# Performance work log

Hardware: AMD Instinct MI355X
Metric: run time of the kernel (lower is better)

Reference implementation:

```python
import jax, jax.numpy as jnp
import numpy as np

N_NODES = 50000
N_EDGES = 800000
D = 64
H = 128


def setup_inputs() -> dict:
    key = jax.random.key(0)
    ks = jax.random.split(key, 6)
    x = jax.random.normal(ks[0], (N_NODES, D), dtype=jnp.float32)
    edge_index = jax.random.randint(ks[1], (2, N_EDGES), 0, N_NODES, dtype=jnp.int64)
    # GIN MLP params (Linear(D->H) -> ReLU -> Linear(H->D))
    W1 = jax.random.normal(ks[2], (D, H), dtype=jnp.float32) * (1.0 / np.sqrt(D))
    b1 = jnp.zeros((H,), dtype=jnp.float32)
    W2 = jax.random.normal(ks[3], (H, D), dtype=jnp.float32) * (1.0 / np.sqrt(H))
    b2 = jnp.zeros((D,), dtype=jnp.float32)
    eps = jnp.zeros((1, 1), dtype=jnp.float32)  # trainable eps parameter
    return {"x": x, "W1": W1, "b1": b1, "W2": W2, "b2": b2, "eps": eps,
            "edge_index": edge_index}


def reference(x, W1, b1, W2, b2, eps, edge_index):
    src, dst = edge_index[0], edge_index[1]
    # node -> edge gather (0th-order ptensor on each edge = sum of endpoint feats)
    msg = x[src] + x[dst]                                    # [E, D]
    # edge -> node gather: each node sums messages of its incident edges
    agg = (jax.ops.segment_sum(msg, src, num_segments=N_NODES)
           + jax.ops.segment_sum(msg, dst, num_segments=N_NODES))  # [N, D]
    ones = jnp.ones((N_EDGES,), dtype=x.dtype)
    deg = (jax.ops.segment_sum(ones, src, num_segments=N_NODES)
           + jax.ops.segment_sum(ones, dst, num_segments=N_NODES))  # [N]
    # subtract deg*x so aggregation reduces to the plain neighbor sum (GIN)
    neighbor = agg - x * deg[:, None]
    out = (1.0 + eps) * x + neighbor                          # eps is [1,1], broadcasts
    # GIN MLP
    h = jax.nn.relu(out @ W1 + b1)
    return h @ W2 + b2
```

## Files before the change

kernel.cpp:

```cpp
#include <hip/hip_runtime.h>


#define D 64
#define H 128
#define MPW 8
#define REGSH 6
#define REGSZ 64
#define P1_BLOCKS 256
#define EVBUF_SZ 6400
#define NR_MAX 1024
#define NCAP 96

typedef __attribute__((ext_vector_type(8))) short short8;
typedef __attribute__((ext_vector_type(4))) float float4v;

__device__ __forceinline__ float lane_bcast(float v, int l) {
    return __uint_as_float(__builtin_amdgcn_readlane(__float_as_uint(v), l));
}

__device__ __forceinline__ unsigned short f2bf(float f) {
    unsigned int u = __float_as_uint(f);
    u = (u + (((u >> 16) & 1u) + 0x7fffu)) >> 16;
    return (unsigned short)u;
}

__device__ __forceinline__ void bf2_acc(unsigned int u, float& a, float& b) {
    a += __uint_as_float(u << 16);
    b += __uint_as_float(u & 0xffff0000u);
}

__global__ void zero_int_kernel(int* __restrict__ p, int n) {
    int i = blockIdx.x * blockDim.x + threadIdx.x;
    if (i < n) p[i] = 0;
}

__global__ void zero_f_kernel(float* __restrict__ p, int n) {
    int i = blockIdx.x * blockDim.x + threadIdx.x;
    if (i < n) p[i] = 0.0f;
}

__global__ void prep_kernel(const float* __restrict__ x,
                            unsigned int* __restrict__ xh2, int npairs,
                            int* __restrict__ cursor, int NR, int CAPB,
                            const float* __restrict__ W1,
                            const float* __restrict__ W2,
                            unsigned short* __restrict__ wsW1,
                            unsigned short* __restrict__ wsW2) {
    int i = blockIdx.x * blockDim.x + threadIdx.x;
    int gs = gridDim.x * blockDim.x;
    for (int k = i; k < npairs; k += gs) {
        float2 v = *(const float2*)(x + (size_t)k * 2);
        unsigned int a = __float_as_uint(v.x);
        unsigned int b = __float_as_uint(v.y);
        a = (a + (((a >> 16) & 1u) + 0x7fffu)) >> 16;
        b = (b + (((b >> 16) & 1u) + 0x7fffu)) >> 16;
        xh2[k] = a | (b << 16);
    }
    if (i < NR) cursor[i] = i * CAPB;
    if (i < 32) xh2[npairs + i] = 0;
    if (i < 8192) {
        int j = i & 7, ln = (i >> 3) & 63;
        int q = (ln >> 4) & 3;
        int tt1 = (i >> 9) & 7, s1 = i >> 12;
        wsW1[i] = f2bf(W1[(s1 * 32 + q * 8 + j) * H + tt1 * 16 + (ln & 15)]);
        int tt2 = (i >> 9) & 3, s2 = i >> 11;
        wsW2[i] = f2bf(W2[(s2 * 32 + q * 8 + j) * D + tt2 * 16 + (ln & 15)]);
    }
}

__global__ __launch_bounds__(256) void part1_kernel(
    const int* __restrict__ src, const int* __restrict__ dst,
    int* __restrict__ cursor, unsigned int* __restrict__ evarr,
    int E, int N, int NR, int CAPB, int EPB)
{
    __shared__ unsigned int evbuf[EVBUF_SZ];
    __shared__ int hist[NR_MAX];
    int t = threadIdx.x;
    for (int b = t; b < NR; b += 256) hist[b] = 0;
    __syncthreads();

    int e0 = blockIdx.x * EPB;
    int ne = E - e0; if (ne > EPB) ne = EPB; if (ne < 0) ne = 0;
    for (int i = t; i < ne; i += 256) {
        int s = src[e0 + i], d = dst[e0 + i];
        s = (s < 0) ? 0 : ((s >= N) ? N - 1 : s);
        d = (d < 0) ? 0 : ((d >= N) ? N - 1 : d);
        evbuf[2 * i]     = ((unsigned int)s << 16) | (unsigned int)d;
        evbuf[2 * i + 1] = ((unsigned int)d << 16) | (unsigned int)s;
        atomicAdd(&hist[s >> REGSH], 1);
        atomicAdd(&hist[d >> REGSH], 1);
    }
    __syncthreads();

    for (int b = t; b < NR; b += 256) {
        int c = hist[b];
        hist[b] = c ? atomicAdd(&cursor[b], c) : 0;
    }
    __syncthreads();

    int nev = 2 * ne;
    for (int i = t; i < nev; i += 256) {
        unsigned int ev = evbuf[i];
        int b = (int)(ev >> (16 + REGSH));
        int slot = atomicAdd(&hist[b], 1);
        if (slot < (b + 1) * CAPB) evarr[slot] = ev;
    }
}

__global__ __launch_bounds__(512) void part2_kernel(
    const unsigned int* __restrict__ evarr, const int* __restrict__ cursor,
    const unsigned short* __restrict__ xh, const float* __restrict__ x,
    const float* __restrict__ epsp, float* __restrict__ pre, int N, int CAPB)
{
    __shared__ unsigned short nbuf[REGSZ * NCAP + 32];
    __shared__ int scnt[REGSZ];
    int t = threadIdx.x;
    int b = blockIdx.x;
    if (t < REGSZ) scnt[t] = 0;
    __syncthreads();

    int base = b * CAPB;
    int count = cursor[b] - base;
    if (count < 0) count = 0;
    if (count > CAPB) count = CAPB;

    for (int i = t; i < count; i += 512) {
        unsigned int ev = evarr[base + i];
        int row = (int)((ev >> 16) & (REGSZ - 1));
        int k = atomicAdd(&scnt[row], 1);
        if (k < NCAP) nbuf[row * NCAP + k] = (unsigned short)(ev & 0xffffu);
    }
    __syncthreads();

    int wave = t >> 6, lane = t & 63;
    int r = lane >> 5;
    int h = lane & 31;
    float e1 = 1.0f + epsp[0];

    for (int k = 0; k < 8; ++k) {
        int n = wave * 8 + k;
        int v = b * REGSZ + n;
        if (v >= N) break;
        int m = scnt[n]; m = (m > NCAP) ? NCAP : m;
        float f0 = 0.0f, f1 = 0.0f;
        for (int j = 0; j < m; j += 32) {
            int cc[16];
#pragma unroll
            for (int q = 0; q < 16; ++q) {
                int ii = j + 2 * q + r;
                int c = (int)nbuf[n * NCAP + ii];
                cc[q] = (ii < m) ? c : N;
            }
            unsigned int u[16];
#pragma unroll
            for (int q = 0; q < 16; ++q)
                u[q] = *(const unsigned int*)(xh + (size_t)cc[q] * D + 2 * h);
#pragma unroll
            for (int q = 0; q < 16; ++q) bf2_acc(u[q], f0, f1);
        }
        f0 += __shfl_xor(f0, 32, 64);
        f1 += __shfl_xor(f1, 32, 64);
        if (r == 0) {
            float2 sv = *(const float2*)(x + (size_t)v * D + 2 * h);
            float2 o;
            o.x = f0 + e1 * sv.x;
            o.y = f1 + e1 * sv.y;
            *(float2*)(pre + (size_t)v * D + 2 * h) = o;
        }
    }
}

__global__ __launch_bounds__(1024) void mlp_mfma(
    const float* __restrict__ pre,
    const unsigned short* __restrict__ wsW1,
    const unsigned short* __restrict__ wsW2,
    const float* __restrict__ b1, const float* __restrict__ b2,
    float* __restrict__ y, int N)
{
    __shared__ unsigned short sW1[8192];
    __shared__ unsigned short sW2[8192];
    __shared__ unsigned short hbuf[16 * 2048];
    int t = threadIdx.x;
    if (t < 1024) {
        ((uint4*)sW1)[t] = ((const uint4*)wsW1)[t];
        ((uint4*)sW2)[t] = ((const uint4*)wsW2)[t];
    }
    __syncthreads();

    int wave = t >> 6, lane = t & 63;
    int quad = lane >> 4, lm = lane & 15;
    int v0 = (blockIdx.x * 16 + wave) * 16;
    int vA = v0 + lm;

    short8 a1[2];
#pragma unroll
    for (int s = 0; s < 2; ++s) {
        float4v p0 = {0.f, 0.f, 0.f, 0.f}, p1 = {0.f, 0.f, 0.f, 0.f};
        if (vA < N) {
            const float* rp = pre + (size_t)vA * D + s * 32 + quad * 8;
            p0 = *(const float4v*)rp;
            p1 = *(const float4v*)(rp + 4);
        }
        short8 a;
        a[0] = (short)f2bf(p0[0]); a[1] = (short)f2bf(p0[1]);
        a[2] = (short)f2bf(p0[2]); a[3] = (short)f2bf(p0[3]);
        a[4] = (short)f2bf(p1[0]); a[5] = (short)f2bf(p1[1]);
        a[6] = (short)f2bf(p1[2]); a[7] = (short)f2bf(p1[3]);
        a1[s] = a;
    }

    float4v acc1[8];
#pragma unroll
    for (int tt = 0; tt < 8; ++tt) {
        float bb = b1[tt * 16 + lm];
        float4v c = {bb, bb, bb, bb};
#pragma unroll
        for (int s = 0; s < 2; ++s) {
            short8 bw = *(const short8*)&sW1[((s * 8 + tt) * 64 + lane) * 8];
            c = __builtin_amdgcn_mfma_f32_16x16x32_bf16(a1[s], bw, c, 0, 0, 0);
        }
        acc1[tt] = c;
    }

    unsigned short* hb = &hbuf[wave * 2048];
#pragma unroll
    for (int tt = 0; tt < 8; ++tt) {
#pragma unroll
        for (int r = 0; r < 4; ++r) {
            float hv = fmaxf(acc1[tt][r], 0.0f);
            hb[(quad * 4 + r) * H + tt * 16 + lm] = f2bf(hv);
        }
    }

    short8 a2[4];
#pragma unroll
    for (int s = 0; s < 4; ++s)
        a2[s] = *(const short8*)&hb[lm * H + s * 32 + quad * 8];

#pragma unroll
    for (int tt = 0; tt < 4; ++tt) {
        float bb = b2[tt * 16 + lm];
        float4v c = {bb, bb, bb, bb};
#pragma unroll
        for (int s = 0; s < 4; ++s) {
            short8 bw = *(const short8*)&sW2[((s * 4 + tt) * 64 + lane) * 8];
            c = __builtin_amdgcn_mfma_f32_16x16x32_bf16(a2[s], bw, c, 0, 0, 0);
        }
#pragma unroll
        for (int r = 0; r < 4; ++r) {
            int v = v0 + quad * 4 + r;
            if (v < N) y[(size_t)v * D + tt * 16 + lm] = c[r];
        }
    }
}


__global__ void count_kernel(const int* __restrict__ ei, int* __restrict__ deg,
                             int twoE, int N) {
    int i = blockIdx.x * blockDim.x + threadIdx.x;
    if (i < twoE) {
        int v = ei[i];
        v = (v < 0) ? 0 : ((v >= N) ? N - 1 : v);
        atomicAdd(&deg[v], 1);
    }
}

__global__ __launch_bounds__(256) void scan_part1(const int* __restrict__ deg,
                                                  int* __restrict__ bsum, int n) {
    __shared__ int red[256];
    int t = threadIdx.x;
    int i = blockIdx.x * 256 + t;
    red[t] = (i < n) ? deg[i] : 0;
    __syncthreads();
    for (int off = 128; off > 0; off >>= 1) {
        if (t < off) red[t] += red[t + off];
        __syncthreads();
    }
    if (t == 0) bsum[blockIdx.x] = red[0];
}

__global__ __launch_bounds__(256) void scan_part2(const int* __restrict__ bsum,
                                                  int* __restrict__ boff,
                                                  int* __restrict__ rowstart_n, int nb) {
    __shared__ int s[256];
    int t = threadIdx.x;
    int v = (t < nb) ? bsum[t] : 0;
    s[t] = v;
    __syncthreads();
    for (int off = 1; off < 256; off <<= 1) {
        int u = (t >= off) ? s[t - off] : 0;
        __syncthreads();
        s[t] += u;
        __syncthreads();
    }
    if (t < nb) boff[t] = s[t] - v;
    if (t == 255) *rowstart_n = s[255];
}

__global__ __launch_bounds__(256) void scan_part3(const int* __restrict__ deg,
                                                  const int* __restrict__ boff,
                                                  int* __restrict__ rowstart,
                                                  int* __restrict__ cursor, int n) {
    __shared__ int s[256];
    int t = threadIdx.x;
    int i = blockIdx.x * 256 + t;
    int v = (i < n) ? deg[i] : 0;
    s[t] = v;
    __syncthreads();
    for (int off = 1; off < 256; off <<= 1) {
        int u = (t >= off) ? s[t - off] : 0;
        __syncthreads();
        s[t] += u;
        __syncthreads();
    }
    if (i < n) {
        int r = boff[blockIdx.x] + s[t] - v;
        rowstart[i] = r;
        cursor[i] = r;
    }
}

__global__ __launch_bounds__(256) void scan_single(const int* __restrict__ deg,
                                                   int* __restrict__ rowstart,
                                                   int* __restrict__ cursor,
                                                   int n, int chunk) {
    __shared__ int psum[256];
    int t = threadIdx.x;
    int lo = t * chunk;
    int hi = lo + chunk; if (hi > n) hi = n;
    int s = 0;
    for (int i = lo; i < hi; ++i) s += deg[i];
    psum[t] = s;
    __syncthreads();
    for (int off = 1; off < 256; off <<= 1) {
        int v = (t >= off) ? psum[t - off] : 0;
        __syncthreads();
        psum[t] += v;
        __syncthreads();
    }
    int run = (t == 0) ? 0 : psum[t - 1];
    for (int i = lo; i < hi; ++i) {
        int d = deg[i];
        rowstart[i] = run;
        cursor[i] = run;
        run += d;
    }
    if (t == 255) rowstart[n] = psum[255];
}

__global__ __launch_bounds__(256) void fill_xcd(
    const int* __restrict__ src, const int* __restrict__ dst,
    int* __restrict__ cursor, int* __restrict__ col,
    int E, int N, int npg)
{
    int grp = blockIdx.x & 7;
    int slice = blockIdx.x >> 3;
    int lo = grp * npg;
    int hi = lo + npg; if (hi > N) hi = N;
    int stride = (gridDim.x >> 3) * 256;
    for (int i = slice * 256 + threadIdx.x; i < E; i += stride) {
        int s = src[i], d = dst[i];
        s = (s < 0) ? 0 : ((s >= N) ? N - 1 : s);
        d = (d < 0) ? 0 : ((d >= N) ? N - 1 : d);
        if (s >= lo && s < hi) { int p = atomicAdd(&cursor[s], 1); col[p] = d; }
        if (d >= lo && d < hi) { int q = atomicAdd(&cursor[d], 1); col[q] = s; }
    }
}

__global__ __launch_bounds__(256) void gather_csr2(
    const float* __restrict__ x, const float* __restrict__ epsp,
    const int* __restrict__ rowstart, const int* __restrict__ col,
    float* __restrict__ pre, int N)
{
    int wid = (blockIdx.x * 256 + threadIdx.x) >> 6;
    int lane = threadIdx.x & 63;
    int v0 = wid * 2;
    if (v0 >= N) return;
    int v1 = v0 + 1;
    float eps1 = 1.0f + epsp[0];
    int j0 = rowstart[v0], re0 = rowstart[v0 + 1];
    float a0 = eps1 * x[(size_t)v0 * D + lane];
    int j1 = 0, re1 = 0;
    float a1 = 0.0f;
    if (v1 < N) {
        j1 = rowstart[v1]; re1 = rowstart[v1 + 1];
        a1 = eps1 * x[(size_t)v1 * D + lane];
    }
    while (j0 + 8 <= re0 && j1 + 8 <= re1) {
        float p0 = x[(size_t)col[j0 + 0] * D + lane];
        float p1 = x[(size_t)col[j0 + 1] * D + lane];
        float p2 = x[(size_t)col[j0 + 2] * D + lane];
        float p3 = x[(size_t)col[j0 + 3] * D + lane];
        float p4 = x[(size_t)col[j0 + 4] * D + lane];
        float p5 = x[(size_t)col[j0 + 5] * D + lane];
        float p6 = x[(size_t)col[j0 + 6] * D + lane];
        float p7 = x[(size_t)col[j0 + 7] * D + lane];
        float q0 = x[(size_t)col[j1 + 0] * D + lane];
        float q1 = x[(size_t)col[j1 + 1] * D + lane];
        float q2 = x[(size_t)col[j1 + 2] * D + lane];
        float q3 = x[(size_t)col[j1 + 3] * D + lane];
        float q4 = x[(size_t)col[j1 + 4] * D + lane];
        float q5 = x[(size_t)col[j1 + 5] * D + lane];
        float q6 = x[(size_t)col[j1 + 6] * D + lane];
        float q7 = x[(size_t)col[j1 + 7] * D + lane];
        a0 += ((p0 + p1) + (p2 + p3)) + ((p4 + p5) + (p6 + p7));
        a1 += ((q0 + q1) + (q2 + q3)) + ((q4 + q5) + (q6 + q7));
        j0 += 8; j1 += 8;
    }
    for (; j0 + 8 <= re0; j0 += 8) {
        float p0 = x[(size_t)col[j0 + 0] * D + lane];
        float p1 = x[(size_t)col[j0 + 1] * D + lane];
        float p2 = x[(size_t)col[j0 + 2] * D + lane];
        float p3 = x[(size_t)col[j0 + 3] * D + lane];
        float p4 = x[(size_t)col[j0 + 4] * D + lane];
        float p5 = x[(size_t)col[j0 + 5] * D + lane];
        float p6 = x[(size_t)col[j0 + 6] * D + lane];
        float p7 = x[(size_t)col[j0 + 7] * D + lane];
        a0 += ((p0 + p1) + (p2 + p3)) + ((p4 + p5) + (p6 + p7));
    }
    for (; j1 + 8 <= re1; j1 += 8) {
        float q0 = x[(size_t)col[j1 + 0] * D + lane];
        float q1 = x[(size_t)col[j1 + 1] * D + lane];
        float q2 = x[(size_t)col[j1 + 2] * D + lane];
        float q3 = x[(size_t)col[j1 + 3] * D + lane];
        float q4 = x[(size_t)col[j1 + 4] * D + lane];
        float q5 = x[(size_t)col[j1 + 5] * D + lane];
        float q6 = x[(size_t)col[j1 + 6] * D + lane];
        float q7 = x[(size_t)col[j1 + 7] * D + lane];
        a1 += ((q0 + q1) + (q2 + q3)) + ((q4 + q5) + (q6 + q7));
    }
    for (; j0 < re0; ++j0) a0 += x[(size_t)col[j0] * D + lane];
    for (; j1 < re1; ++j1) a1 += x[(size_t)col[j1] * D + lane];
    pre[(size_t)v0 * D + lane] = a0;
    if (v1 < N) pre[(size_t)v1 * D + lane] = a1;
}

__device__ __forceinline__ void mlp_store(
    const float* acc, float* sW, int v0, int t, int lane, int nNodes,
    const float* __restrict__ W2,
    const float* __restrict__ b1, const float* __restrict__ b2,
    float* __restrict__ y)
{
    float b1a = b1[lane], b1b = b1[lane + 64];
    float ha[MPW], hb[MPW];
#pragma unroll
    for (int m = 0; m < MPW; ++m) { ha[m] = b1a; hb[m] = b1b; }
#pragma unroll 4
    for (int f = 0; f < D; ++f) {
        float wa = sW[f * H + lane];
        float wb = sW[f * H + lane + 64];
#pragma unroll
        for (int m = 0; m < MPW; ++m) {
            float o = lane_bcast(acc[m], f);
            ha[m] += o * wa;
            hb[m] += o * wb;
        }
    }
#pragma unroll
    for (int m = 0; m < MPW; ++m) {
        ha[m] = fmaxf(ha[m], 0.0f);
        hb[m] = fmaxf(hb[m], 0.0f);
    }

    __syncthreads();
    for (int i = t; i < H * D; i += 256) sW[i] = W2[i];
    __syncthreads();

    float b2v = b2[lane];
    float yv[MPW];
#pragma unroll
    for (int m = 0; m < MPW; ++m) yv[m] = b2v;
#pragma unroll 4
    for (int k = 0; k < 64; ++k) {
        float w = sW[k * D + lane];
#pragma unroll
        for (int m = 0; m < MPW; ++m) yv[m] += lane_bcast(ha[m], k) * w;
    }
#pragma unroll 4
    for (int k = 0; k < 64; ++k) {
        float w = sW[(k + 64) * D + lane];
#pragma unroll
        for (int m = 0; m < MPW; ++m) yv[m] += lane_bcast(hb[m], k) * w;
    }
#pragma unroll
    for (int m = 0; m < MPW; ++m) {
        int v = v0 + m;
        if (v < nNodes) y[(size_t)v * D + lane] = yv[m];
    }
}

__global__ __launch_bounds__(256) void mlp_pre(
    const float* __restrict__ pre, const float* __restrict__ W1,
    const float* __restrict__ b1, const float* __restrict__ W2,
    const float* __restrict__ b2, float* __restrict__ y, int nNodes)
{
    __shared__ float sW[D * H];
    int t = threadIdx.x;
    for (int i = t; i < D * H; i += 256) sW[i] = W1[i];
    __syncthreads();
    int wave = t >> 6, lane = t & 63;
    int v0 = (blockIdx.x * 4 + wave) * MPW;
    float acc[MPW];
#pragma unroll
    for (int m = 0; m < MPW; ++m) {
        int v = v0 + m;
        acc[m] = (v < nNodes) ? pre[(size_t)v * D + lane] : 0.0f;
    }
    mlp_store(acc, sW, v0, t, lane, nNodes, W2, b1, b2, y);
}

__global__ __launch_bounds__(256) void gather_mlp_csr(
    const float* __restrict__ x, const float* __restrict__ W1,
    const float* __restrict__ b1, const float* __restrict__ W2,
    const float* __restrict__ b2, const float* __restrict__ epsp,
    const int* __restrict__ rowstart, const int* __restrict__ col,
    float* __restrict__ y, int nNodes)
{
    __shared__ float sW[D * H];
    int t = threadIdx.x;
    for (int i = t; i < D * H; i += 256) sW[i] = W1[i];
    __syncthreads();
    int wave = t >> 6, lane = t & 63;
    float eps1 = 1.0f + epsp[0];
    int v0 = (blockIdx.x * 4 + wave) * MPW;
    float acc[MPW];
#pragma unroll
    for (int m = 0; m < MPW; ++m) {
        int v = v0 + m;
        float a = 0.0f;
        if (v < nNodes) {
            int rs = rowstart[v], re = rowstart[v + 1];
            a = eps1 * x[(size_t)v * D + lane];
            int j = rs;
            for (; j + 8 <= re; j += 8) {
                float p0 = x[(size_t)col[j + 0] * D + lane];
                float p1 = x[(size_t)col[j + 1] * D + lane];
                float p2 = x[(size_t)col[j + 2] * D + lane];
                float p3 = x[(size_t)col[j + 3] * D + lane];
                float p4 = x[(size_t)col[j + 4] * D + lane];
                float p5 = x[(size_t)col[j + 5] * D + lane];
                float p6 = x[(size_t)col[j + 6] * D + lane];
                float p7 = x[(size_t)col[j + 7] * D + lane];
                a += ((p0 + p1) + (p2 + p3)) + ((p4 + p5) + (p6 + p7));
            }
            for (; j < re; ++j) a += x[(size_t)col[j] * D + lane];
        }
        acc[m] = a;
    }
    mlp_store(acc, sW, v0, t, lane, nNodes, W2, b1, b2, y);
}

__global__ void scatter_kernel(const float* __restrict__ x,
                               const int* __restrict__ src,
                               const int* __restrict__ dst,
                               float* __restrict__ agg, int E, int N)
{
    int tid = blockIdx.x * blockDim.x + threadIdx.x;
    int e = tid >> 6, lane = tid & 63;
    if (e < E) {
        int s = src[e], d = dst[e];
        s = (s < 0) ? 0 : ((s >= N) ? N - 1 : s);
        d = (d < 0) ? 0 : ((d >= N) ? N - 1 : d);
        float xs = x[(size_t)s * D + lane];
        float xd = x[(size_t)d * D + lane];
        atomicAdd(&agg[(size_t)s * D + lane], xd);
        atomicAdd(&agg[(size_t)d * D + lane], xs);
    }
}

__global__ __launch_bounds__(256) void mlp_from_agg(
    const float* __restrict__ x, const float* __restrict__ W1,
    const float* __restrict__ b1, const float* __restrict__ W2,
    const float* __restrict__ b2, const float* __restrict__ epsp,
    float* __restrict__ yio, int nNodes)
{
    __shared__ float sW[D * H];
    int t = threadIdx.x;
    for (int i = t; i < D * H; i += 256) sW[i] = W1[i];
    __syncthreads();
    int wave = t >> 6, lane = t & 63;
    float eps1 = 1.0f + epsp[0];
    int v0 = (blockIdx.x * 4 + wave) * MPW;
    float acc[MPW];
#pragma unroll
    for (int m = 0; m < MPW; ++m) {
        int v = v0 + m;
        acc[m] = (v < nNodes)
                   ? (eps1 * x[(size_t)v * D + lane] + yio[(size_t)v * D + lane])
                   : 0.0f;
    }
    mlp_store(acc, sW, v0, t, lane, nNodes, W2, b1, b2, yio);
}

extern "C" void kernel_launch(void* const* d_in, const int* in_sizes, int n_in,
                              void* d_out, int out_size, void* d_ws, size_t ws_size,
                              hipStream_t stream)
{
    const float* x   = (const float*)d_in[0];
    const float* W1  = (const float*)d_in[1];
    const float* b1  = (const float*)d_in[2];
    const float* W2  = (const float*)d_in[3];
    const float* b2  = (const float*)d_in[4];
    const float* eps = (const float*)d_in[5];
    const int*   ei  = (const int*)d_in[6];
    float* out = (float*)d_out;

    int N = in_sizes[0] / D;
    int E = in_sizes[6] / 2;
    const int* src = ei;
    const int* dst = ei + E;

    int nb = (N + 255) / 256;

    int NR = (N + REGSZ - 1) >> REGSH;
    int meanE = (NR > 0) ? (2 * E + NR - 1) / NR : 0;
    int CAPB = meanE + meanE / 4 + 128;
    int EPB = (E + P1_BLOCKS - 1) / P1_BLOCKS;
    size_t off_cur  = 0;
    size_t off_ev   = (off_cur + (size_t)NR * 4 + 15) & ~(size_t)15;
    size_t off_xh   = (off_ev + (size_t)NR * CAPB * 4 + 15) & ~(size_t)15;
    size_t off_w1   = (off_xh + (size_t)(N + 1) * D * 2 + 15) & ~(size_t)15;
    size_t off_w2   = off_w1 + 8192 * 2;
    size_t need_part = off_w2 + 8192 * 2;

    size_t csr_ints = (size_t)(3 * N + 1 + 2 * E) + 512;
    size_t need_csr = csr_ints * sizeof(int);
    size_t need_split = need_csr + (size_t)N * D * sizeof(float);
    int mlp_blocks = (N + 4 * MPW - 1) / (4 * MPW);

    if (ws_size >= need_part && N >= REGSZ && N <= 65535
        && NR <= NR_MAX && 2 * EPB <= EVBUF_SZ && (N * D) % 2 == 0) {
        char* base = (char*)d_ws;
        int*            cursor = (int*)(base + off_cur);
        unsigned int*   evarr  = (unsigned int*)(base + off_ev);
        unsigned short* xh     = (unsigned short*)(base + off_xh);
        unsigned short* wsW1   = (unsigned short*)(base + off_w1);
        unsigned short* wsW2   = (unsigned short*)(base + off_w2);
        float*          pre    = out;
        int npairs = N * D / 2;

        prep_kernel<<<1024, 256, 0, stream>>>(
            x, (unsigned int*)xh, npairs, cursor, NR, CAPB, W1, W2, wsW1, wsW2);
        part1_kernel<<<P1_BLOCKS, 256, 0, stream>>>(
            src, dst, cursor, evarr, E, N, NR, CAPB, EPB);
        part2_kernel<<<NR, 512, 0, stream>>>(
            evarr, cursor, xh, x, eps, pre, N, CAPB);
        int mfma_blocks = (N + 255) / 256;
        mlp_mfma<<<mfma_blocks, 1024, 0, stream>>>(pre, wsW1, wsW2, b1, b2, out, N);
    } else if (ws_size >= need_csr) {
        int*   deg      = (int*)d_ws;
        int*   cursor   = deg + N;
        int*   rowstart = cursor + N;
        int*   col      = rowstart + (N + 1);
        int*   bsum     = col + 2 * E;
        int*   boff     = bsum + 256;
        float* pre      = (float*)(boff + 256);

        zero_int_kernel<<<(N + 255) / 256, 256, 0, stream>>>(deg, N);
        count_kernel<<<(2 * E + 255) / 256, 256, 0, stream>>>(ei, deg, 2 * E, N);
        if (nb <= 256) {
            scan_part1<<<nb, 256, 0, stream>>>(deg, bsum, N);
            scan_part2<<<1, 256, 0, stream>>>(bsum, boff, &rowstart[N], nb);
            scan_part3<<<nb, 256, 0, stream>>>(deg, boff, rowstart, cursor, N);
        } else {
            int chunk = (N + 255) / 256;
            scan_single<<<1, 256, 0, stream>>>(deg, rowstart, cursor, N, chunk);
        }
        fill_xcd<<<2048, 256, 0, stream>>>(src, dst, cursor, col, E, N, (N + 7) / 8);
        int waves = (N + 1) / 2;
        int gather_blocks = (waves + 3) / 4;
        if (ws_size >= need_split) {
            gather_csr2<<<gather_blocks, 256, 0, stream>>>(x, eps, rowstart, col, pre, N);
            mlp_pre<<<mlp_blocks, 256, 0, stream>>>(pre, W1, b1, W2, b2, out, N);
        } else {
            gather_mlp_csr<<<mlp_blocks, 256, 0, stream>>>(
                x, W1, b1, W2, b2, eps, rowstart, col, out, N);
        }
    } else {
        int nd = N * D;
        zero_f_kernel<<<(nd + 255) / 256, 256, 0, stream>>>(out, nd);
        long long st = (long long)E * 64;
        scatter_kernel<<<(int)((st + 255) / 256), 256, 0, stream>>>(x, src, dst, out, E, N);
        mlp_from_agg<<<mlp_blocks, 256, 0, stream>>>(x, W1, b1, W2, b2, eps, out, N);
    }
}
```

Baseline: 148.9 us.

## Fuse MLP into aggregation kernel and move bf16 conversion into partition kernel

The GIN MLP is now run inside the aggregation kernel. Each block keeps its 64 aggregated node rows in LDS and applies the two MFMA layers there, so the fp32 'pre' tensor no longer makes a round trip through global memory and one launch is gone. The x-to-bf16 conversion moves from the prep kernel into part1, so prep runs with a small grid. In exchange, each block now uses much more LDS (weights, hbuf and pre tile), which may lower occupancy of the gather phase, and every block reloads the weight tiles.

```diff
diff --git a/kernel.cpp b/kernel.cpp
--- a/kernel.cpp
+++ b/kernel.cpp
@@ -10,6 +10,7 @@
 #define EVBUF_SZ 6400
 #define NR_MAX 1024
 #define NCAP 96
+#define PSTR 68
 
 typedef __attribute__((ext_vector_type(8))) short short8;
 typedef __attribute__((ext_vector_type(4))) float float4v;
@@ -39,23 +40,13 @@
     if (i < n) p[i] = 0.0f;
 }
 
-__global__ void prep_kernel(const float* __restrict__ x,
-                            unsigned int* __restrict__ xh2, int npairs,
+__global__ void prep_kernel(unsigned int* __restrict__ xh2, int npairs,
                             int* __restrict__ cursor, int NR, int CAPB,
                             const float* __restrict__ W1,
                             const float* __restrict__ W2,
                             unsigned short* __restrict__ wsW1,
                             unsigned short* __restrict__ wsW2) {
     int i = blockIdx.x * blockDim.x + threadIdx.x;
-    int gs = gridDim.x * blockDim.x;
-    for (int k = i; k < npairs; k += gs) {
-        float2 v = *(const float2*)(x + (size_t)k * 2);
-        unsigned int a = __float_as_uint(v.x);
-        unsigned int b = __float_as_uint(v.y);
-        a = (a + (((a >> 16) & 1u) + 0x7fffu)) >> 16;
-        b = (b + (((b >> 16) & 1u) + 0x7fffu)) >> 16;
-        xh2[k] = a | (b << 16);
-    }
     if (i < NR) cursor[i] = i * CAPB;
     if (i < 32) xh2[npairs + i] = 0;
     if (i < 8192) {
@@ -71,11 +62,23 @@
 __global__ __launch_bounds__(256) void part1_kernel(
     const int* __restrict__ src, const int* __restrict__ dst,
     int* __restrict__ cursor, unsigned int* __restrict__ evarr,
+    const float* __restrict__ x, unsigned int* __restrict__ xh2, int npairs,
     int E, int N, int NR, int CAPB, int EPB)
 {
     __shared__ unsigned int evbuf[EVBUF_SZ];
     __shared__ int hist[NR_MAX];
     int t = threadIdx.x;
+
+    int gstride = gridDim.x * 256;
+    for (int i = blockIdx.x * 256 + t; i < npairs; i += gstride) {
+        float2 v = *(const float2*)(x + (size_t)i * 2);
+        unsigned int a = __float_as_uint(v.x);
+        unsigned int b = __float_as_uint(v.y);
+        a = (a + (((a >> 16) & 1u) + 0x7fffu)) >> 16;
+        b = (b + (((b >> 16) & 1u) + 0x7fffu)) >> 16;
+        xh2[i] = a | (b << 16);
+    }
+
     for (int b = t; b < NR; b += 256) hist[b] = 0;
     __syncthreads();
 
@@ -107,16 +110,29 @@
     }
 }
 
-__global__ __launch_bounds__(512) void part2_kernel(
+__global__ __launch_bounds__(512) void part2_fused(
     const unsigned int* __restrict__ evarr, const int* __restrict__ cursor,
     const unsigned short* __restrict__ xh, const float* __restrict__ x,
-    const float* __restrict__ epsp, float* __restrict__ pre, int N, int CAPB)
+    const float* __restrict__ epsp,
+    const unsigned short* __restrict__ wsW1,
+    const unsigned short* __restrict__ wsW2,
+    const float* __restrict__ b1, const float* __restrict__ b2,
+    float* __restrict__ y, int N, int CAPB)
 {
     __shared__ unsigned short nbuf[REGSZ * NCAP + 32];
     __shared__ int scnt[REGSZ];
+    __shared__ float pre_lds[REGSZ * PSTR];
+    __shared__ unsigned short sW1[8192];
+    __shared__ unsigned short sW2[8192];
+    __shared__ unsigned short hbuf[4 * 16 * H];
     int t = threadIdx.x;
     int b = blockIdx.x;
     if (t < REGSZ) scnt[t] = 0;
+#pragma unroll
+    for (int i = 0; i < 2; ++i) {
+        ((uint4*)sW1)[t + i * 512] = ((const uint4*)wsW1)[t + i * 512];
+        ((uint4*)sW2)[t + i * 512] = ((const uint4*)wsW2)[t + i * 512];
+    }
     __syncthreads();
 
     int base = b * CAPB;
@@ -140,8 +156,8 @@
     for (int k = 0; k < 8; ++k) {
         int n = wave * 8 + k;
         int v = b * REGSZ + n;
-        if (v >= N) break;
-        int m = scnt[n]; m = (m > NCAP) ? NCAP : m;
+        int m = (v < N) ? scnt[n] : 0;
+        m = (m > NCAP) ? NCAP : m;
         float f0 = 0.0f, f1 = 0.0f;
         for (int j = 0; j < m; j += 32) {
             int cc[16];
@@ -161,46 +177,24 @@
         f0 += __shfl_xor(f0, 32, 64);
         f1 += __shfl_xor(f1, 32, 64);
         if (r == 0) {
-            float2 sv = *(const float2*)(x + (size_t)v * D + 2 * h);
-            float2 o;
-            o.x = f0 + e1 * sv.x;
-            o.y = f1 + e1 * sv.y;
-            *(float2*)(pre + (size_t)v * D + 2 * h) = o;
-        }
-    }
-}
-
-__global__ __launch_bounds__(1024) void mlp_mfma(
-    const float* __restrict__ pre,
-    const unsigned short* __restrict__ wsW1,
-    const unsigned short* __restrict__ wsW2,
-    const float* __restrict__ b1, const float* __restrict__ b2,
-    float* __restrict__ y, int N)
-{
-    __shared__ unsigned short sW1[8192];
-    __shared__ unsigned short sW2[8192];
-    __shared__ unsigned short hbuf[16 * 2048];
-    int t = threadIdx.x;
-    if (t < 1024) {
-        ((uint4*)sW1)[t] = ((const uint4*)wsW1)[t];
-        ((uint4*)sW2)[t] = ((const uint4*)wsW2)[t];
-    }
-    __syncthreads();
-
-    int wave = t >> 6, lane = t & 63;
+            float2 sv = make_float2(0.0f, 0.0f);
+            if (v < N) sv = *(const float2*)(x + (size_t)v * D + 2 * h);
+            pre_lds[n * PSTR + 2 * h]     = f0 + e1 * sv.x;
+            pre_lds[n * PSTR + 2 * h + 1] = f1 + e1 * sv.y;
+        }
+    }
+    __syncthreads();
+
+    int p = wave >> 1, hh = wave & 1;
     int quad = lane >> 4, lm = lane & 15;
-    int v0 = (blockIdx.x * 16 + wave) * 16;
-    int vA = v0 + lm;
+    int row0 = p * 16 + lm;
 
     short8 a1[2];
 #pragma unroll
     for (int s = 0; s < 2; ++s) {
-        float4v p0 = {0.f, 0.f, 0.f, 0.f}, p1 = {0.f, 0.f, 0.f, 0.f};
-        if (vA < N) {
-            const float* rp = pre + (size_t)vA * D + s * 32 + quad * 8;
-            p0 = *(const float4v*)rp;
-            p1 = *(const float4v*)(rp + 4);
-        }
+        const float* rp = &pre_lds[row0 * PSTR + s * 32 + quad * 8];
+        float4v p0 = *(const float4v*)rp;
+        float4v p1 = *(const float4v*)(rp + 4);
         short8 a;
         a[0] = (short)f2bf(p0[0]); a[1] = (short)f2bf(p0[1]);
         a[2] = (short)f2bf(p0[2]); a[3] = (short)f2bf(p0[3]);
@@ -209,9 +203,10 @@
         a1[s] = a;
     }
 
-    float4v acc1[8];
-#pragma unroll
-    for (int tt = 0; tt < 8; ++tt) {
+    float4v acc1[4];
+#pragma unroll
+    for (int i = 0; i < 4; ++i) {
+        int tt = hh * 4 + i;
         float bb = b1[tt * 16 + lm];
         float4v c = {bb, bb, bb, bb};
 #pragma unroll
@@ -219,26 +214,30 @@
             short8 bw = *(const short8*)&sW1[((s * 8 + tt) * 64 + lane) * 8];
             c = __builtin_amdgcn_mfma_f32_16x16x32_bf16(a1[s], bw, c, 0, 0, 0);
         }
-        acc1[tt] = c;
-    }
-
-    unsigned short* hb = &hbuf[wave * 2048];
-#pragma unroll
-    for (int tt = 0; tt < 8; ++tt) {
-#pragma unroll
-        for (int r = 0; r < 4; ++r) {
-            float hv = fmaxf(acc1[tt][r], 0.0f);
-            hb[(quad * 4 + r) * H + tt * 16 + lm] = f2bf(hv);
-        }
-    }
+        acc1[i] = c;
+    }
+
+    unsigned short* hb = &hbuf[p * 16 * H];
+#pragma unroll
+    for (int i = 0; i < 4; ++i) {
+        int tt = hh * 4 + i;
+#pragma unroll
+        for (int rr = 0; rr < 4; ++rr) {
+            float hv = fmaxf(acc1[i][rr], 0.0f);
+            hb[(quad * 4 + rr) * H + tt * 16 + lm] = f2bf(hv);
+        }
+    }
+    __syncthreads();
 
     short8 a2[4];
 #pragma unroll
     for (int s = 0; s < 4; ++s)
         a2[s] = *(const short8*)&hb[lm * H + s * 32 + quad * 8];
 
-#pragma unroll
-    for (int tt = 0; tt < 4; ++tt) {
+    int v0t = b * REGSZ + p * 16;
+#pragma unroll
+    for (int i = 0; i < 2; ++i) {
+        int tt = hh * 2 + i;
         float bb = b2[tt * 16 + lm];
         float4v c = {bb, bb, bb, bb};
 #pragma unroll
@@ -247,9 +246,9 @@
             c = __builtin_amdgcn_mfma_f32_16x16x32_bf16(a2[s], bw, c, 0, 0, 0);
         }
 #pragma unroll
-        for (int r = 0; r < 4; ++r) {
-            int v = v0 + quad * 4 + r;
-            if (v < N) y[(size_t)v * D + tt * 16 + lm] = c[r];
+        for (int rr = 0; rr < 4; ++rr) {
+            int v = v0t + quad * 4 + rr;
+            if (v < N) y[(size_t)v * D + tt * 16 + lm] = c[rr];
         }
     }
 }
@@ -636,17 +635,15 @@
         unsigned short* xh     = (unsigned short*)(base + off_xh);
         unsigned short* wsW1   = (unsigned short*)(base + off_w1);
         unsigned short* wsW2   = (unsigned short*)(base + off_w2);
-        float*          pre    = out;
         int npairs = N * D / 2;
 
-        prep_kernel<<<1024, 256, 0, stream>>>(
-            x, (unsigned int*)xh, npairs, cursor, NR, CAPB, W1, W2, wsW1, wsW2);
+        prep_kernel<<<32, 256, 0, stream>>>(
+            (unsigned int*)xh, npairs, cursor, NR, CAPB, W1, W2, wsW1, wsW2);
         part1_kernel<<<P1_BLOCKS, 256, 0, stream>>>(
-            src, dst, cursor, evarr, E, N, NR, CAPB, EPB);
-        part2_kernel<<<NR, 512, 0, stream>>>(
-            evarr, cursor, xh, x, eps, pre, N, CAPB);
-        int mfma_blocks = (N + 255) / 256;
-        mlp_mfma<<<mfma_blocks, 1024, 0, stream>>>(pre, wsW1, wsW2, b1, b2, out, N);
+            src, dst, cursor, evarr, x, (unsigned int*)xh, npairs,
+            E, N, NR, CAPB, EPB);
+        part2_fused<<<NR, 512, 0, stream>>>(
+            evarr, cursor, xh, x, eps, wsW1, wsW2, b1, b2, out, N, CAPB);
     } else if (ws_size >= need_csr) {
         int*   deg      = (int*)d_ws;
         int*   cursor   = deg + N;
```

Result: no change. 150.0 us (+0.8%).
